# Optimization experiments

Hardware: AMD Instinct MI355X
Metric: run time of the kernel (lower is better)

Reference implementation:

```python
import jax, jax.numpy as jnp
import numpy as np

B, S, D = 4, 2048, 1024
H = 16
HD = D // H  # 64

def setup_inputs() -> dict:
    key = jax.random.key(0)
    k1, k2, k3 = jax.random.split(key, 3)
    x = jax.random.normal(k1, (B, S, D), dtype=jnp.float32)
    w_qkv = jax.random.normal(k2, (D, 3 * D), dtype=jnp.float32) * 0.02
    w_proj = jax.random.normal(k3, (D, D), dtype=jnp.float32) * 0.02
    return {"x": x, "w_qkv": w_qkv, "w_proj": w_proj}

def reference(x, w_qkv, w_proj):
    b, s, d = x.shape
    qkv = x @ w_qkv                                  # [b,s,3d]
    q, k, v = jnp.split(qkv, 3, axis=2)
    # [b,s,d] -> [b,h,s,hd]
    q = q.reshape(b, s, H, HD).transpose(0, 2, 1, 3)
    k = k.reshape(b, s, H, HD).transpose(0, 2, 1, 3)
    v = v.reshape(b, s, H, HD).transpose(0, 2, 1, 3)
    att = jnp.einsum('bhqd,bhkd->bhqk', q, k) / jnp.sqrt(jnp.float32(HD))
    causal = jnp.tril(jnp.ones((s, s), dtype=bool))
    att = jnp.where(causal[None, None], att, jnp.float32(-jnp.inf))
    att = jax.nn.softmax(att, axis=-1)
    y = jnp.einsum('bhqk,bhkd->bhqd', att, v)        # [b,h,s,hd]
    y = y.transpose(0, 2, 1, 3).reshape(b, s, d)
    return y @ w_proj
```

## Files before the change

### kernel.cpp

```cpp
#include <hip/hip_runtime.h>
#include <stdint.h>

typedef unsigned short u16;
typedef unsigned int u32;
typedef __attribute__((ext_vector_type(8))) short bf16x8;
typedef __attribute__((ext_vector_type(4))) float f32x4;
typedef __attribute__((ext_vector_type(16))) float f32x16;

__device__ __forceinline__ u16 f2bf(float f) {
  union { float f; unsigned u; } v; v.f = f;
  unsigned r = v.u + 0x7fffu + ((v.u >> 16) & 1u);
  return (u16)(r >> 16);
}

__device__ __forceinline__ u32 pk_bf16(float lo, float hi) {
  u32 r;
  asm("v_cvt_pk_bf16_f32 %0, %1, %2" : "=v"(r) : "v"(lo), "v"(hi));
  return r;
}
#define PLSWAP(a, b) asm volatile("v_permlane32_swap_b32 %0, %1" : "+v"(a), "+v"(b))

__device__ __forceinline__ void async_copy16(u16* lds_dst, const u16* g_src) {
  __builtin_amdgcn_global_load_lds(
      (const __attribute__((address_space(1))) unsigned*)(g_src),
      (__attribute__((address_space(3))) unsigned*)(lds_dst),
      16, 0, 0);
}

#define MFMA16(a, b, c) __builtin_amdgcn_mfma_f32_16x16x32_bf16((a), (b), (c), 0, 0, 0)
#define MFMA32(a, b, c) __builtin_amdgcn_mfma_f32_32x32x16_bf16((a), (b), (c), 0, 0, 0)

#define QSCALE 0.18033688011112042f

__global__ void cvt_bf16_kernel(const float* __restrict__ in, u16* __restrict__ out, int n4) {
  int i = blockIdx.x * blockDim.x + threadIdx.x;
  int stride = gridDim.x * blockDim.x;
  for (; i < n4; i += stride) {
    float4 v = ((const float4*)in)[i];
    ushort4 o;
    o.x = f2bf(v.x); o.y = f2bf(v.y); o.z = f2bf(v.z); o.w = f2bf(v.w);
    ((ushort4*)out)[i] = o;
  }
}

__global__ void transpose_cvt_kernel(const float* __restrict__ in, u16* __restrict__ out,
                                     int R, int C) {
  __shared__ float tile[32][33];
  int bx = blockIdx.x * 32;
  int by = blockIdx.y * 32;
  int tx = threadIdx.x & 31, ty = threadIdx.x >> 5;
#pragma unroll
  for (int j = 0; j < 32; j += 8)
    tile[ty + j][tx] = in[(size_t)(by + ty + j) * C + bx + tx];
  __syncthreads();
#pragma unroll
  for (int j = 0; j < 32; j += 8)
    out[(size_t)(bx + ty + j) * R + by + tx] = f2bf(tile[tx][ty + j]);
}

template<int MODE>
__global__ __launch_bounds__(256, 2)
void gemm_cnt(const u16* __restrict__ A, const u16* __restrict__ BT,
              int K, int N,
              u16* __restrict__ q_o, u16* __restrict__ k_o, u16* __restrict__ vt_o,
              float* __restrict__ f_o) {
  __shared__ u16 As[2][128 * 64];
  __shared__ u16 Bs[2][128 * 64];

  const int t = threadIdx.x;
  const int w = t >> 6, l = t & 63;
  const int lr = l & 15, g = l >> 4;
  const int wm = (w >> 1) * 64, wn = (w & 1) * 64;
  const int m0 = blockIdx.x * 128, n0 = blockIdx.y * 128;

  const int r = t >> 3;
  const int sw = ((t & 7) * 16) ^ ((r & 7) << 4);
  const u16* pA = A + (size_t)(m0 + r) * K + (sw >> 1);
  const u16* pB = BT + (size_t)(n0 + r) * K + (sw >> 1);

#define STG(buf, kk)                                                    \
  do {                                                                  \
    async_copy16(&As[buf][t * 8],        pA + (kk));                    \
    async_copy16(&As[buf][2048 + t * 8], pA + (size_t)32 * K + (kk));   \
    async_copy16(&As[buf][4096 + t * 8], pA + (size_t)64 * K + (kk));   \
    async_copy16(&As[buf][6144 + t * 8], pA + (size_t)96 * K + (kk));   \
    async_copy16(&Bs[buf][t * 8],        pB + (kk));                    \
    async_copy16(&Bs[buf][2048 + t * 8], pB + (size_t)32 * K + (kk));   \
    async_copy16(&Bs[buf][4096 + t * 8], pB + (size_t)64 * K + (kk));   \
    async_copy16(&Bs[buf][6144 + t * 8], pB + (size_t)96 * K + (kk));   \
  } while (0)

  f32x4 acc[4][4] = {};

  STG(0, 0);

  const int NTt = K / 64;
  for (int T = 0; T < NTt; ++T) {
    const int cur = T & 1;
    if (T + 1 < NTt) {
      STG(cur ^ 1, (T + 1) * 64);
      asm volatile("s_waitcnt vmcnt(8)" ::: "memory");
    } else {
      asm volatile("s_waitcnt vmcnt(0)" ::: "memory");
    }
    __builtin_amdgcn_sched_barrier(0);
    asm volatile("s_barrier" ::: "memory");

    bf16x8 af[4][2], bfr[4][2];
#pragma unroll
    for (int mf = 0; mf < 4; ++mf)
#pragma unroll
      for (int ks = 0; ks < 2; ++ks) {
        const int row = wm + mf * 16 + lr;
        af[mf][ks] = *(const bf16x8*)&As[cur][row * 64 + (((ks * 64 + g * 16) ^ ((row & 7) << 4)) >> 1)];
      }
#pragma unroll
    for (int nf = 0; nf < 4; ++nf)
#pragma unroll
      for (int ks = 0; ks < 2; ++ks) {
        const int row = wn + nf * 16 + lr;
        bfr[nf][ks] = *(const bf16x8*)&Bs[cur][row * 64 + (((ks * 64 + g * 16) ^ ((row & 7) << 4)) >> 1)];
      }
#pragma unroll
    for (int mf = 0; mf < 4; ++mf)
#pragma unroll
      for (int nf = 0; nf < 4; ++nf) {
        acc[mf][nf] = MFMA16(af[mf][0], bfr[nf][0], acc[mf][nf]);
        acc[mf][nf] = MFMA16(af[mf][1], bfr[nf][1], acc[mf][nf]);
      }
    asm volatile("s_barrier" ::: "memory");
  }
#undef STG

#pragma unroll
  for (int mf = 0; mf < 4; ++mf) {
#pragma unroll
    for (int nf = 0; nf < 4; ++nf) {
      const int col = n0 + wn + nf * 16 + lr;
#pragma unroll
      for (int j = 0; j < 4; ++j) {
        const int rowc = m0 + wm + mf * 16 + g * 4 + j;
        const float v = acc[mf][nf][j];
        if (MODE == 0) {
          const int which = col >> 10, rr = col & 1023;
          const int h = rr >> 6, hd = rr & 63;
          const int b = rowc >> 11, s = rowc & 2047;
          const size_t bh = (size_t)b * 16 + h;
          if (which == 0)      q_o[(bh * 2048 + s) * 64 + hd] = f2bf(v * QSCALE);
          else if (which == 1) k_o[(bh * 2048 + s) * 64 + hd] = f2bf(v);
          else                 vt_o[(bh * 64 + hd) * 2048 + s] = f2bf(v);
        } else {
          f_o[(size_t)rowc * N + col] = v;
        }
      }
    }
  }
}

__global__ __launch_bounds__(256, 4)
void attn_kernel(const u16* __restrict__ qws, const u16* __restrict__ kws,
                 const u16* __restrict__ vtws, u16* __restrict__ ybf) {
  __shared__ u16 Ksh[2][64 * 64];
  __shared__ u16 VTsh[2][64 * 64];

  const int bh = blockIdx.x & 63;
  const int gq = blockIdx.x >> 6, a2 = gq & 3, b2 = gq >> 2;
  const int qtile = (b2 == 0) ? 15 - a2 : (b2 == 1) ? 8 + a2 : (b2 == 2) ? 4 + a2 : 3 - a2;
  const int t = threadIdx.x;
  const int w = t >> 6, l = t & 63;
  const int lq = l & 31;
  const int h = l >> 5;
  const int q0 = qtile * 128 + w * 32;
  const int qg = q0 + lq;

  bf16x8 qf[4];
  {
    const u16* qb = qws + ((size_t)bh * 2048 + qg) * 64 + h * 8;
#pragma unroll
    for (int s = 0; s < 4; ++s) qf[s] = *(const bf16x8*)(qb + s * 16);
  }

  f32x16 oacc[2] = {};
  float lsum = 0.f;

  const int srow = t >> 3;
  const int ssw = ((t & 7) * 16) ^ ((srow & 7) << 4);
  const u16* kb0 = kws + ((size_t)bh * 2048 + srow) * 64 + (ssw >> 1);
  const u16* vb0 = vtws + ((size_t)bh * 64 + srow) * 2048 + (ssw >> 1);

#define STAGE(kv0, buf)                                                \
  do {                                                                 \
    async_copy16(&Ksh[buf][t * 8],          kb0 + (size_t)(kv0)*64);   \
    async_copy16(&Ksh[buf][(t + 256) * 8],  kb0 + (size_t)((kv0)+32)*64); \
    async_copy16(&VTsh[buf][t * 8],         vb0 + (kv0));              \
    async_copy16(&VTsh[buf][(t + 256) * 8], vb0 + (size_t)32*2048 + (kv0)); \
  } while (0)

  const int nt = (qtile + 1) * 2;
  STAGE(0, 0);

  for (int ti = 0; ti < nt; ++ti) {
    const int kv0 = ti * 64;
    const int cur = ti & 1;
    if (ti + 1 < nt) {
      STAGE((ti + 1) * 64, cur ^ 1);
      asm volatile("s_waitcnt vmcnt(4)" ::: "memory");
    } else {
      asm volatile("s_waitcnt vmcnt(0)" ::: "memory");
    }
    __builtin_amdgcn_sched_barrier(0);
    asm volatile("s_barrier" ::: "memory");

    if (kv0 <= q0 + 31) {
      const u16* Kc = Ksh[cur];
      const u16* Vc = VTsh[cur];

      f32x16 st[2] = {};
      __builtin_amdgcn_s_setprio(1);
#pragma unroll
      for (int kt = 0; kt < 2; ++kt) {
        const int krow = kt * 32 + lq;
        const int swz = (krow & 7) << 4;
#pragma unroll
        for (int s = 0; s < 4; ++s) {
          bf16x8 kf = *(const bf16x8*)&Kc[krow * 64 + (((s * 32 + h * 16) ^ swz) >> 1)];
          st[kt] = MFMA32(kf, qf[s], st[kt]);
        }
      }
      __builtin_amdgcn_s_setprio(0);

      const bool diag = (kv0 + 63 > q0);
#pragma unroll
      for (int kt = 0; kt < 2; ++kt)
#pragma unroll
        for (int p = 0; p < 16; ++p) {
          float e = exp2f(st[kt][p]);
          if (diag) {
            const int key = kv0 + kt * 32 + (p & 3) + 8 * (p >> 2) + 4 * h;
            e = (key <= qg) ? e : 0.f;
          }
          st[kt][p] = e;
          lsum += e;
        }

      bf16x8 pb[4];
#pragma unroll
      for (int kt = 0; kt < 2; ++kt)
#pragma unroll
        for (int s2l = 0; s2l < 2; ++s2l) {
          const int p0 = s2l * 8;
          u32 L0 = pk_bf16(st[kt][p0 + 0], st[kt][p0 + 1]);
          u32 L1 = pk_bf16(st[kt][p0 + 2], st[kt][p0 + 3]);
          u32 H0 = pk_bf16(st[kt][p0 + 4], st[kt][p0 + 5]);
          u32 H1 = pk_bf16(st[kt][p0 + 6], st[kt][p0 + 7]);
          PLSWAP(L0, H0);
          PLSWAP(L1, H1);
          union { u32 u[4]; bf16x8 v; } pw;
          pw.u[0] = L0; pw.u[1] = L1; pw.u[2] = H0; pw.u[3] = H1;
          pb[kt * 2 + s2l] = pw.v;
        }

      __builtin_amdgcn_s_setprio(1);
#pragma unroll
      for (int dt = 0; dt < 2; ++dt) {
        const int vrow = dt * 32 + lq;
        const int swz = (vrow & 7) << 4;
#pragma unroll
        for (int s2 = 0; s2 < 4; ++s2) {
          bf16x8 vf = *(const bf16x8*)&Vc[vrow * 64 + (((s2 * 32 + h * 16) ^ swz) >> 1)];
          oacc[dt] = MFMA32(vf, pb[s2], oacc[dt]);
        }
      }
      __builtin_amdgcn_s_setprio(0);
    }
    asm volatile("s_barrier" ::: "memory");
  }
#undef STAGE

  lsum += __shfl_xor(lsum, 32, 64);
  const float linv = 1.f / lsum;

  const int b = bh >> 4, hh = bh & 15;
  u16* yb = ybf + ((size_t)b * 2048 + qg) * 1024 + hh * 64;
#pragma unroll
  for (int dt = 0; dt < 2; ++dt)
#pragma unroll
    for (int pg = 0; pg < 4; ++pg) {
      u32 w0 = pk_bf16(oacc[dt][pg * 4 + 0] * linv, oacc[dt][pg * 4 + 1] * linv);
      u32 w1 = pk_bf16(oacc[dt][pg * 4 + 2] * linv, oacc[dt][pg * 4 + 3] * linv);
      union { u32 u[2]; unsigned long long ll; } pk2;
      pk2.u[0] = w0; pk2.u[1] = w1;
      *(unsigned long long*)(yb + dt * 32 + 8 * pg + 4 * h) = pk2.ll;
    }
}

extern "C" void kernel_launch(void* const* d_in, const int* in_sizes, int n_in,
                              void* d_out, int out_size, void* d_ws, size_t ws_size,
                              hipStream_t stream) {
  const float* x     = (const float*)d_in[0];
  const float* wqkv  = (const float*)d_in[1];
  const float* wproj = (const float*)d_in[2];
  float* out = (float*)d_out;

  char* ws = (char*)d_ws;
  u16* xbf    = (u16*)ws;
  u16* ybf    = xbf;
  u16* wqkvT  = (u16*)(ws + 16777216);
  u16* wprojT = (u16*)(ws + 16777216 + 6291456);
  u16* qws    = (u16*)(ws + 25165824);
  u16* kws    = (u16*)(ws + 41943040);
  u16* vtws   = (u16*)(ws + 58720256);

  cvt_bf16_kernel<<<2048, 256, 0, stream>>>(x, xbf, (8192 * 1024) / 4);
  transpose_cvt_kernel<<<dim3(3072 / 32, 1024 / 32), 256, 0, stream>>>(wqkv, wqkvT, 1024, 3072);
  transpose_cvt_kernel<<<dim3(1024 / 32, 1024 / 32), 256, 0, stream>>>(wproj, wprojT, 1024, 1024);
  gemm_cnt<0><<<dim3(64, 24), 256, 0, stream>>>(xbf, wqkvT, 1024, 3072, qws, kws, vtws, nullptr);
  attn_kernel<<<16 * 64, 256, 0, stream>>>(qws, kws, vtws, ybf);
  gemm_cnt<1><<<dim3(64, 8), 256, 0, stream>>>(ybf, wprojT, 1024, 1024, nullptr, nullptr, nullptr, out);
}
```

Before: 177.7 us.

## Process two 32-row query blocks per wave to reuse K/V fragments

Doubles the attention query tile from 128 to 256 rows per block. Each wave now handles two 32-query sub-blocks that share each K and V LDS fragment read, which halves the LDS traffic and the global K/V staging per query. The grid drops to 512 blocks with a new heavy-first ordering, and launch bounds relax to 2 blocks per CU to fit the doubled accumulators. The costs are lower occupancy, more register pressure and coarser causal load balance across fewer blocks.

```diff
diff --git a/kernel.cpp b/kernel.cpp
--- a/kernel.cpp
+++ b/kernel.cpp
@@ -157,31 +157,36 @@
   }
 }
 
-__global__ __launch_bounds__(256, 4)
+__global__ __launch_bounds__(256, 2)
 void attn_kernel(const u16* __restrict__ qws, const u16* __restrict__ kws,
                  const u16* __restrict__ vtws, u16* __restrict__ ybf) {
   __shared__ u16 Ksh[2][64 * 64];
   __shared__ u16 VTsh[2][64 * 64];
 
-  const int bh = blockIdx.x & 63;
-  const int gq = blockIdx.x >> 6, a2 = gq & 3, b2 = gq >> 2;
-  const int qtile = (b2 == 0) ? 15 - a2 : (b2 == 1) ? 8 + a2 : (b2 == 2) ? 4 + a2 : 3 - a2;
+  const int bid = blockIdx.x;
+  const int bh = bid & 63;
+  const int g = (bid < 256) ? (7 - (bid >> 6)) : ((bid >> 6) - 4);
+  const int qbase = g * 256;
   const int t = threadIdx.x;
   const int w = t >> 6, l = t & 63;
   const int lq = l & 31;
   const int h = l >> 5;
-  const int q0 = qtile * 128 + w * 32;
-  const int qg = q0 + lq;
-
-  bf16x8 qf[4];
+  const int q0 = qbase + w * 64;
+  const int qgA = q0 + lq, qgB = q0 + 32 + lq;
+
+  bf16x8 qfA[4], qfB[4];
   {
-    const u16* qb = qws + ((size_t)bh * 2048 + qg) * 64 + h * 8;
-#pragma unroll
-    for (int s = 0; s < 4; ++s) qf[s] = *(const bf16x8*)(qb + s * 16);
-  }
-
-  f32x16 oacc[2] = {};
-  float lsum = 0.f;
+    const u16* qa = qws + ((size_t)bh * 2048 + qgA) * 64 + h * 8;
+    const u16* qb = qws + ((size_t)bh * 2048 + qgB) * 64 + h * 8;
+#pragma unroll
+    for (int s = 0; s < 4; ++s) {
+      qfA[s] = *(const bf16x8*)(qa + s * 16);
+      qfB[s] = *(const bf16x8*)(qb + s * 16);
+    }
+  }
+
+  f32x16 oaccA[2] = {}, oaccB[2] = {};
+  float lsumA = 0.f, lsumB = 0.f;
 
   const int srow = t >> 3;
   const int ssw = ((t & 7) * 16) ^ ((srow & 7) << 4);
@@ -196,7 +201,7 @@
     async_copy16(&VTsh[buf][(t + 256) * 8], vb0 + (size_t)32*2048 + (kv0)); \
   } while (0)
 
-  const int nt = (qtile + 1) * 2;
+  const int nt = 4 * (g + 1);
   STAGE(0, 0);
 
   for (int ti = 0; ti < nt; ++ti) {
@@ -211,54 +216,67 @@
     __builtin_amdgcn_sched_barrier(0);
     asm volatile("s_barrier" ::: "memory");
 
-    if (kv0 <= q0 + 31) {
+    if (kv0 <= q0 + 63) {
       const u16* Kc = Ksh[cur];
       const u16* Vc = VTsh[cur];
-
-      f32x16 st[2] = {};
-      __builtin_amdgcn_s_setprio(1);
+      const bool diagA = (kv0 + 63 > q0);
+      const bool diagB = (kv0 + 63 > q0 + 32);
+      bf16x8 pbA[4], pbB[4];
+
 #pragma unroll
       for (int kt = 0; kt < 2; ++kt) {
         const int krow = kt * 32 + lq;
         const int swz = (krow & 7) << 4;
+        f32x16 sa = {}, sb = {};
+        __builtin_amdgcn_s_setprio(1);
 #pragma unroll
         for (int s = 0; s < 4; ++s) {
           bf16x8 kf = *(const bf16x8*)&Kc[krow * 64 + (((s * 32 + h * 16) ^ swz) >> 1)];
-          st[kt] = MFMA32(kf, qf[s], st[kt]);
-        }
-      }
-      __builtin_amdgcn_s_setprio(0);
-
-      const bool diag = (kv0 + 63 > q0);
-#pragma unroll
-      for (int kt = 0; kt < 2; ++kt)
+          sa = MFMA32(kf, qfA[s], sa);
+          sb = MFMA32(kf, qfB[s], sb);
+        }
+        __builtin_amdgcn_s_setprio(0);
+
 #pragma unroll
         for (int p = 0; p < 16; ++p) {
-          float e = exp2f(st[kt][p]);
-          if (diag) {
-            const int key = kv0 + kt * 32 + (p & 3) + 8 * (p >> 2) + 4 * h;
-            e = (key <= qg) ? e : 0.f;
-          }
-          st[kt][p] = e;
-          lsum += e;
-        }
-
-      bf16x8 pb[4];
-#pragma unroll
-      for (int kt = 0; kt < 2; ++kt)
+          const int key = kv0 + kt * 32 + (p & 3) + 8 * (p >> 2) + 4 * h;
+          float ea = exp2f(sa[p]);
+          if (diagA) ea = (key <= qgA) ? ea : 0.f;
+          sa[p] = ea;
+          lsumA += ea;
+          float eb = exp2f(sb[p]);
+          if (diagB) eb = (key <= qgB) ? eb : 0.f;
+          sb[p] = eb;
+          lsumB += eb;
+        }
+
 #pragma unroll
         for (int s2l = 0; s2l < 2; ++s2l) {
           const int p0 = s2l * 8;
-          u32 L0 = pk_bf16(st[kt][p0 + 0], st[kt][p0 + 1]);
-          u32 L1 = pk_bf16(st[kt][p0 + 2], st[kt][p0 + 3]);
-          u32 H0 = pk_bf16(st[kt][p0 + 4], st[kt][p0 + 5]);
-          u32 H1 = pk_bf16(st[kt][p0 + 6], st[kt][p0 + 7]);
-          PLSWAP(L0, H0);
-          PLSWAP(L1, H1);
-          union { u32 u[4]; bf16x8 v; } pw;
-          pw.u[0] = L0; pw.u[1] = L1; pw.u[2] = H0; pw.u[3] = H1;
-          pb[kt * 2 + s2l] = pw.v;
-        }
+          {
+            u32 L0 = pk_bf16(sa[p0 + 0], sa[p0 + 1]);
+            u32 L1 = pk_bf16(sa[p0 + 2], sa[p0 + 3]);
+            u32 H0 = pk_bf16(sa[p0 + 4], sa[p0 + 5]);
+            u32 H1 = pk_bf16(sa[p0 + 6], sa[p0 + 7]);
+            PLSWAP(L0, H0);
+            PLSWAP(L1, H1);
+            union { u32 u[4]; bf16x8 v; } pw;
+            pw.u[0] = L0; pw.u[1] = L1; pw.u[2] = H0; pw.u[3] = H1;
+            pbA[kt * 2 + s2l] = pw.v;
+          }
+          {
+            u32 L0 = pk_bf16(sb[p0 + 0], sb[p0 + 1]);
+            u32 L1 = pk_bf16(sb[p0 + 2], sb[p0 + 3]);
+            u32 H0 = pk_bf16(sb[p0 + 4], sb[p0 + 5]);
+            u32 H1 = pk_bf16(sb[p0 + 6], sb[p0 + 7]);
+            PLSWAP(L0, H0);
+            PLSWAP(L1, H1);
+            union { u32 u[4]; bf16x8 v; } pw;
+            pw.u[0] = L0; pw.u[1] = L1; pw.u[2] = H0; pw.u[3] = H1;
+            pbB[kt * 2 + s2l] = pw.v;
+          }
+        }
+      }
 
       __builtin_amdgcn_s_setprio(1);
 #pragma unroll
@@ -268,7 +286,8 @@
 #pragma unroll
         for (int s2 = 0; s2 < 4; ++s2) {
           bf16x8 vf = *(const bf16x8*)&Vc[vrow * 64 + (((s2 * 32 + h * 16) ^ swz) >> 1)];
-          oacc[dt] = MFMA32(vf, pb[s2], oacc[dt]);
+          oaccA[dt] = MFMA32(vf, pbA[s2], oaccA[dt]);
+          oaccB[dt] = MFMA32(vf, pbB[s2], oaccB[dt]);
         }
       }
       __builtin_amdgcn_s_setprio(0);
@@ -277,20 +296,33 @@
   }
 #undef STAGE
 
-  lsum += __shfl_xor(lsum, 32, 64);
-  const float linv = 1.f / lsum;
+  lsumA += __shfl_xor(lsumA, 32, 64);
+  lsumB += __shfl_xor(lsumB, 32, 64);
+  const float linvA = 1.f / lsumA;
+  const float linvB = 1.f / lsumB;
 
   const int b = bh >> 4, hh = bh & 15;
-  u16* yb = ybf + ((size_t)b * 2048 + qg) * 1024 + hh * 64;
+  u16* ya = ybf + ((size_t)b * 2048 + qgA) * 1024 + hh * 64;
+  u16* yb = ybf + ((size_t)b * 2048 + qgB) * 1024 + hh * 64;
 #pragma unroll
   for (int dt = 0; dt < 2; ++dt)
 #pragma unroll
     for (int pg = 0; pg < 4; ++pg) {
-      u32 w0 = pk_bf16(oacc[dt][pg * 4 + 0] * linv, oacc[dt][pg * 4 + 1] * linv);
-      u32 w1 = pk_bf16(oacc[dt][pg * 4 + 2] * linv, oacc[dt][pg * 4 + 3] * linv);
-      union { u32 u[2]; unsigned long long ll; } pk2;
-      pk2.u[0] = w0; pk2.u[1] = w1;
-      *(unsigned long long*)(yb + dt * 32 + 8 * pg + 4 * h) = pk2.ll;
+      const int doff = dt * 32 + 8 * pg + 4 * h;
+      {
+        u32 w0 = pk_bf16(oaccA[dt][pg * 4 + 0] * linvA, oaccA[dt][pg * 4 + 1] * linvA);
+        u32 w1 = pk_bf16(oaccA[dt][pg * 4 + 2] * linvA, oaccA[dt][pg * 4 + 3] * linvA);
+        union { u32 u[2]; unsigned long long ll; } pk2;
+        pk2.u[0] = w0; pk2.u[1] = w1;
+        *(unsigned long long*)(ya + doff) = pk2.ll;
+      }
+      {
+        u32 w0 = pk_bf16(oaccB[dt][pg * 4 + 0] * linvB, oaccB[dt][pg * 4 + 1] * linvB);
+        u32 w1 = pk_bf16(oaccB[dt][pg * 4 + 2] * linvB, oaccB[dt][pg * 4 + 3] * linvB);
+        union { u32 u[2]; unsigned long long ll; } pk2;
+        pk2.u[0] = w0; pk2.u[1] = w1;
+        *(unsigned long long*)(yb + doff) = pk2.ll;
+      }
     }
 }
 
@@ -315,6 +347,6 @@
   transpose_cvt_kernel<<<dim3(3072 / 32, 1024 / 32), 256, 0, stream>>>(wqkv, wqkvT, 1024, 3072);
   transpose_cvt_kernel<<<dim3(1024 / 32, 1024 / 32), 256, 0, stream>>>(wproj, wprojT, 1024, 1024);
   gemm_cnt<0><<<dim3(64, 24), 256, 0, stream>>>(xbf, wqkvT, 1024, 3072, qws, kws, vtws, nullptr);
-  attn_kernel<<<16 * 64, 256, 0, stream>>>(qws, kws, vtws, ybf);
+  attn_kernel<<<512, 256, 0, stream>>>(qws, kws, vtws, ybf);
   gemm_cnt<1><<<dim3(64, 8), 256, 0, stream>>>(ybf, wprojT, 1024, 1024, nullptr, nullptr, nullptr, out);
 }
```

Measured after the change: 203.3 us. 14.5% more time.
